# Optimization experiments

Measured on AMD Instinct MI355X. Metric: run time of the kernel, lower is better.

## Reference

```python
import jax, jax.numpy as jnp
import numpy as np

DIM = 2048
H = 16       # num_heads
HKV = 4      # num_kv_heads
HD = DIM // H  # head_dim = 128
REP = H // HKV
ROPE_BASE = 10000.0
QK_GAIN_INIT = 1.0
B, T = 4, 2048


def rms_norm(x):
    # F.rms_norm with eps=None -> machine eps of dtype, no weight
    eps = jnp.finfo(x.dtype).eps
    return x * jax.lax.rsqrt(jnp.mean(x * x, axis=-1, keepdims=True) + eps)


def apply_rotary_emb(x, cos, sin):
    # x: [B, h, T, HD]; cos/sin: [T, HD//2]
    h = x.shape[-1] // 2
    x1, x2 = x[..., :h], x[..., h:]
    return jnp.concatenate((x1 * cos + x2 * sin, -x1 * sin + x2 * cos), axis=-1)


def setup_inputs() -> dict:
    key = jax.random.key(0)
    ks = jax.random.split(key, 6)
    kv_dim = HKV * HD
    x = jax.random.normal(ks[0], (B, T, DIM), dtype=jnp.float32)
    Wq = jax.random.normal(ks[1], (DIM, DIM), dtype=jnp.float32) * 0.02
    Wk = jax.random.normal(ks[2], (kv_dim, DIM), dtype=jnp.float32) * 0.02
    Wv = jax.random.normal(ks[3], (kv_dim, DIM), dtype=jnp.float32) * 0.02
    Wproj = jax.random.normal(ks[4], (DIM, DIM), dtype=jnp.float32) * 0.02
    q_gain = jnp.full((H,), QK_GAIN_INIT, dtype=jnp.float32)
    return {"x": x, "Wq": Wq, "Wk": Wk, "Wv": Wv, "Wproj": Wproj, "q_gain": q_gain}


def reference(x, Wq, Wk, Wv, Wproj, q_gain):
    Bs, Ts, D = x.shape
    # QKV projections (bias-free Linear: x @ W.T)
    q = (x @ Wq.T).reshape(Bs, Ts, H, HD).transpose(0, 2, 1, 3)      # [B,H,T,HD]
    k = (x @ Wk.T).reshape(Bs, Ts, HKV, HD).transpose(0, 2, 1, 3)    # [B,HKV,T,HD]
    v = (x @ Wv.T).reshape(Bs, Ts, HKV, HD).transpose(0, 2, 1, 3)
    # RMSNorm over head_dim
    q, k = rms_norm(q), rms_norm(k)
    # rotary
    inv_freq = 1.0 / (ROPE_BASE ** (jnp.arange(0, HD, 2, dtype=jnp.float32) / HD))
    t = jnp.arange(Ts, dtype=jnp.float32)
    freqs = jnp.outer(t, inv_freq)  # [T, HD//2]
    cos, sin = jnp.cos(freqs), jnp.sin(freqs)
    q = apply_rotary_emb(q, cos, sin)
    k = apply_rotary_emb(k, cos, sin)
    # per-head query gain
    q = q * q_gain[None, :, None, None]
    # GQA attention without materializing repeated K/V
    qg = q.reshape(Bs, HKV, REP, Ts, HD)
    scale = 1.0 / jnp.sqrt(jnp.asarray(HD, dtype=q.dtype))
    scores = jnp.einsum('bgrtd,bgsd->bgrts', qg, k) * scale  # [B,HKV,REP,T,T]
    causal = jnp.tril(jnp.ones((Ts, Ts), dtype=bool))
    scores = jnp.where(causal, scores, jnp.finfo(scores.dtype).min)
    attn = jax.nn.softmax(scores, axis=-1)
    y = jnp.einsum('bgrts,bgsd->bgrtd', attn, v)              # [B,HKV,REP,T,HD]
    y = y.reshape(Bs, H, Ts, HD).transpose(0, 2, 1, 3).reshape(Bs, Ts, D)
    return y @ Wproj.T
```

## Files before the change

kernel.cpp:

```cpp
#include <hip/hip_runtime.h>
#include <stdint.h>

typedef unsigned short u16;
typedef __attribute__((ext_vector_type(4))) float f32x4;
typedef __attribute__((ext_vector_type(8))) __bf16 bf16x8;
typedef __attribute__((ext_vector_type(4))) u16 u16x4;
typedef __attribute__((ext_vector_type(8))) u16 u16x8;

#define T_SEQ 2048
#define NB 4
#define NH 16
#define NKV 4
#define HDIM 128
#define PSTR 72

__device__ __forceinline__ u16 f2bf(float f) {
  __bf16 h = (__bf16)f;
  return __builtin_bit_cast(u16, h);
}
__device__ __forceinline__ float bf2f(u16 u) {
  union { uint32_t u; float f; } v; v.u = ((uint32_t)u) << 16;
  return v.f;
}
__device__ __forceinline__ void gload16(const void* g, void* l) {
  __builtin_amdgcn_global_load_lds((const __attribute__((address_space(1))) void*)g,
                                   (__attribute__((address_space(3))) void*)l, 16, 0, 0);
}
__device__ __forceinline__ f32x4 mfma16(bf16x8 a, bf16x8 b, f32x4 c) {
  return __builtin_amdgcn_mfma_f32_16x16x32_bf16(a, b, c, 0, 0, 0);
}

__global__ __launch_bounds__(256) void cvt_bf16(const float* __restrict__ in,
                                                u16* __restrict__ out, int n) {
  int idx = blockIdx.x * 256 + threadIdx.x;
  int stride = gridDim.x * 256;
  for (int i = idx * 4; i < n; i += stride * 4) {
    f32x4 v = *(const f32x4*)(in + i);
    u16x4 o;
    o[0] = f2bf(v[0]); o[1] = f2bf(v[1]); o[2] = f2bf(v[2]); o[3] = f2bf(v[3]);
    *(u16x4*)(out + i) = o;
  }
}

template <int MODE>
__global__ __launch_bounds__(256) void gemm128p3(const u16* __restrict__ A,
                                                 const u16* __restrict__ Bt,
                                                 u16* __restrict__ q_o, u16* __restrict__ k_o,
                                                 u16* __restrict__ v_o, float* __restrict__ f_o,
                                                 int K, int nx, int cpx) {
  __shared__ __align__(16) u16 As3[3 * 128 * 32];
  __shared__ __align__(16) u16 Bs3[3 * 128 * 32];
  const int tid = threadIdx.x;
  const int l = tid & 63, w = tid >> 6;
  const int l15 = l & 15, g16 = l >> 4;
  const int wr = w >> 1, wc = w & 1;

  const int oid = blockIdx.x + nx * blockIdx.y;
  const int wid = (oid & 7) * cpx + (oid >> 3);
  const int m0 = (wid / nx) * 128, n0 = (wid % nx) * 128;

  f32x4 acc[4][4] = {};

  const int row0 = tid >> 2, row1 = 64 + (tid >> 2), cc = tid & 3;
  const int sc0 = cc ^ ((row0 >> 1) & 3), sc1 = cc ^ ((row1 >> 1) & 3);
  const u16* pA0 = A + (size_t)(m0 + row0) * K + sc0 * 8;
  const u16* pA1 = A + (size_t)(m0 + row1) * K + sc1 * 8;
  const u16* pB0 = Bt + (size_t)(n0 + row0) * K + sc0 * 8;
  const u16* pB1 = Bt + (size_t)(n0 + row1) * K + sc1 * 8;

#define STAGE(buf)                                                   \
  {                                                                  \
    char* ab = (char*)As3 + (buf) * 8192 + w * 1024;                 \
    char* bb = (char*)Bs3 + (buf) * 8192 + w * 1024;                 \
    gload16(pA0, ab);                                                \
    gload16(pA1, ab + 4096);                                         \
    gload16(pB0, bb);                                                \
    gload16(pB1, bb + 4096);                                         \
    pA0 += 32; pA1 += 32; pB0 += 32; pB1 += 32;                      \
  }

#define COMPUTE(buf)                                                 \
  {                                                                  \
    const u16* AsB = As3 + (buf) * 4096;                             \
    const u16* BsB = Bs3 + (buf) * 4096;                             \
    bf16x8 af[4], bfr[4];                                            \
    _Pragma("unroll")                                                \
    for (int mt = 0; mt < 4; ++mt) {                                 \
      int arow = wr * 64 + mt * 16 + l15;                            \
      af[mt] = *(const bf16x8*)&AsB[arow * 32 +                      \
                                    ((g16 ^ ((arow >> 1) & 3)) * 8)];\
    }                                                                \
    _Pragma("unroll")                                                \
    for (int nt = 0; nt < 4; ++nt) {                                 \
      int brow = wc * 64 + nt * 16 + l15;                            \
      bfr[nt] = *(const bf16x8*)&BsB[brow * 32 +                     \
                                     ((g16 ^ ((brow >> 1) & 3)) * 8)];\
    }                                                                \
    __builtin_amdgcn_s_setprio(1);                                   \
    _Pragma("unroll")                                                \
    for (int mt = 0; mt < 4; ++mt)                                   \
      _Pragma("unroll")                                              \
      for (int nt = 0; nt < 4; ++nt)                                 \
        acc[mt][nt] = mfma16(af[mt], bfr[nt], acc[mt][nt]);          \
    __builtin_amdgcn_s_setprio(0);                                   \
  }

  const int ntiles = K >> 5;
  STAGE(0);
  STAGE(1);
  asm volatile("s_waitcnt vmcnt(4)" ::: "memory");
  __builtin_amdgcn_s_barrier();

  int cur = 0, nxt = 2;
  for (int t = 0; t < ntiles; ++t) {
    const bool more2 = (t + 2 < ntiles);
    if (more2) STAGE(nxt);
    COMPUTE(cur);
    if (t + 1 < ntiles) {
      if (more2) {
        asm volatile("s_waitcnt vmcnt(4)" ::: "memory");
      } else {
        asm volatile("s_waitcnt vmcnt(0)" ::: "memory");
      }
      __builtin_amdgcn_s_barrier();
    }
    cur = (cur == 2) ? 0 : cur + 1;
    nxt = (nxt == 2) ? 0 : nxt + 1;
  }
#undef STAGE
#undef COMPUTE

#pragma unroll
  for (int mt = 0; mt < 4; ++mt) {
#pragma unroll
    for (int r = 0; r < 4; ++r) {
      int row = m0 + wr * 64 + mt * 16 + g16 * 4 + r;
#pragma unroll
      for (int nt = 0; nt < 4; ++nt) {
        int n = n0 + wc * 64 + nt * 16 + l15;
        float val = acc[mt][nt][r];
        if (MODE == 1) {
          f_o[(size_t)row * 2048 + n] = val;
        } else {
          int b = row >> 11, t = row & (T_SEQ - 1);
          u16 bv = f2bf(val);
          if (n < 2048) {
            int h = n >> 7, d = n & 127;
            q_o[((size_t)(b * NH + h) * T_SEQ + t) * HDIM + d] = bv;
          } else if (n < 2560) {
            int n2 = n - 2048; int h = n2 >> 7, d = n2 & 127;
            k_o[((size_t)(b * NKV + h) * T_SEQ + t) * HDIM + d] = bv;
          } else {
            int n2 = n - 2560; int h = n2 >> 7, d = n2 & 127;
            v_o[((size_t)(b * NKV + h) * T_SEQ + t) * HDIM + d] = bv;
          }
        }
      }
    }
  }
}

template <int MODE>
__global__ __launch_bounds__(512, 2) void gemm256(const u16* __restrict__ A,
                                                  const u16* __restrict__ Bt,
                                                  u16* __restrict__ q_o, u16* __restrict__ k_o,
                                                  u16* __restrict__ v_o, float* __restrict__ f_o,
                                                  int K, int ntn, int cpx) {
  __shared__ __align__(16) u16 As[2][256 * 64];
  __shared__ __align__(16) u16 Bs[2][256 * 64];
  const int tid = threadIdx.x;
  const int l = tid & 63, w = tid >> 6;
  const int l16 = l & 15, g16 = l >> 4;
  const int wr = w >> 2, wc = w & 3;

  const int oid = blockIdx.x;
  const int wid = (oid & 7) * cpx + (oid >> 3);
  const int m0 = (wid / ntn) * 256, n0 = (wid % ntn) * 256;

  f32x4 acc[8][4] = {};

  const int srow = tid >> 3, scc = tid & 7;
  const u16* pA[4];
  const u16* pB[4];
#pragma unroll
  for (int j = 0; j < 4; ++j) {
    int row = j * 64 + srow;
    int cc = scc ^ (row & 7);
    pA[j] = A + (size_t)(m0 + row) * K + cc * 8;
    pB[j] = Bt + (size_t)(n0 + row) * K + cc * 8;
  }

#define STAGE(buf)                                              \
  {                                                             \
    char* ab = (char*)As[buf] + w * 1024;                       \
    char* bb = (char*)Bs[buf] + w * 1024;                       \
    _Pragma("unroll")                                           \
    for (int j = 0; j < 4; ++j) {                               \
      gload16(pA[j], ab + j * 8192);                            \
      pA[j] += 64;                                              \
    }                                                           \
    _Pragma("unroll")                                           \
    for (int j = 0; j < 4; ++j) {                               \
      gload16(pB[j], bb + j * 8192);                            \
      pB[j] += 64;                                              \
    }                                                           \
  }

  const int ntk = K >> 6;
  STAGE(0);
  __syncthreads();

  for (int t = 0; t < ntk; ++t) {
    const int buf = t & 1;
    if (t + 1 < ntk) STAGE(buf ^ 1);
#pragma unroll
    for (int ks = 0; ks < 2; ++ks) {
      bf16x8 bfr[4];
#pragma unroll
      for (int nf = 0; nf < 4; ++nf) {
        int brow = wc * 64 + nf * 16 + l16;
        int slot = (ks * 4 + g16) ^ (brow & 7);
        bfr[nf] = *(const bf16x8*)&Bs[buf][brow * 64 + slot * 8];
      }
#pragma unroll
      for (int rh = 0; rh < 2; ++rh) {
        bf16x8 af[4];
#pragma unroll
        for (int f = 0; f < 4; ++f) {
          int arow = wr * 128 + rh * 64 + f * 16 + l16;
          int slot = (ks * 4 + g16) ^ (arow & 7);
          af[f] = *(const bf16x8*)&As[buf][arow * 64 + slot * 8];
        }
        __builtin_amdgcn_s_setprio(1);
#pragma unroll
        for (int f = 0; f < 4; ++f)
#pragma unroll
          for (int nf = 0; nf < 4; ++nf)
            acc[rh * 4 + f][nf] = mfma16(af[f], bfr[nf], acc[rh * 4 + f][nf]);
        __builtin_amdgcn_s_setprio(0);
      }
    }
    __syncthreads();
  }
#undef STAGE

#pragma unroll
  for (int rf = 0; rf < 8; ++rf) {
#pragma unroll
    for (int rr = 0; rr < 4; ++rr) {
      int row = m0 + wr * 128 + rf * 16 + g16 * 4 + rr;
#pragma unroll
      for (int nf = 0; nf < 4; ++nf) {
        int n = n0 + wc * 64 + nf * 16 + l16;
        float val = acc[rf][nf][rr];
        if (MODE == 1) {
          f_o[(size_t)row * 2048 + n] = val;
        } else {
          int b = row >> 11, t = row & (T_SEQ - 1);
          u16 bv = f2bf(val);
          if (n < 2048) {
            int h = n >> 7, d = n & 127;
            q_o[((size_t)(b * NH + h) * T_SEQ + t) * HDIM + d] = bv;
          } else if (n < 2560) {
            int n2 = n - 2048; int h = n2 >> 7, d = n2 & 127;
            k_o[((size_t)(b * NKV + h) * T_SEQ + t) * HDIM + d] = bv;
          } else {
            int n2 = n - 2560; int h = n2 >> 7, d = n2 & 127;
            v_o[((size_t)(b * NKV + h) * T_SEQ + t) * HDIM + d] = bv;
          }
        }
      }
    }
  }
}

__global__ __launch_bounds__(256) void rmsrope(u16* __restrict__ buf,
                                               const float* __restrict__ gains,
                                               int nheads, float fold, int useGain) {
  const int w = threadIdx.x >> 6, l = threadIdx.x & 63;
  const int rid = blockIdx.x * 4 + w;
  const int t = rid & (T_SEQ - 1);
  const int h = (rid >> 11) % nheads;
  u16* p = buf + (size_t)rid * HDIM;
  float x1 = bf2f(p[l]), x2 = bf2f(p[l + 64]);
  float ss = x1 * x1 + x2 * x2;
#pragma unroll
  for (int m = 32; m; m >>= 1) ss += __shfl_xor(ss, m, 64);
  float rn = rsqrtf(ss * (1.0f / 128.0f) + 1.1920928955078125e-7f);
  float g = useGain ? gains[h] * fold : fold;
  float sc = rn * g;
  float inv = exp2f(-(float)l * (13.287712379549449f / 64.0f));
  float ang = (float)t * inv;
  float s, c;
  __sincosf(ang, &s, &c);
  float o1 = (x1 * c + x2 * s) * sc;
  float o2 = (x2 * c - x1 * s) * sc;
  p[l] = f2bf(o1);
  p[l + 64] = f2bf(o2);
}

__global__ __launch_bounds__(256) void vtrans(const u16* __restrict__ in,
                                              u16* __restrict__ out) {
  __shared__ u16 tileT[64][PSTR];
  const int tid = threadIdx.x;
  const int t0 = blockIdx.x * 64, d0 = blockIdx.y * 64, bg = blockIdx.z;
  const int row = tid >> 2, c0 = (tid & 3) * 16;
  const u16* src = in + ((size_t)bg * T_SEQ + t0 + row) * HDIM + d0 + c0;
  u16x8 a = *(const u16x8*)src;
  u16x8 bb = *(const u16x8*)(src + 8);
#pragma unroll
  for (int j = 0; j < 8; ++j) {
    tileT[c0 + j][row] = a[j];
    tileT[c0 + 8 + j][row] = bb[j];
  }
  __syncthreads();
  u16* dst = out + ((size_t)bg * HDIM + d0 + row) * T_SEQ + t0 + c0;
  *(u16x8*)dst = *(const u16x8*)&tileT[row][c0];
  *(u16x8*)(dst + 8) = *(const u16x8*)&tileT[row][c0 + 8];
}

__global__ __launch_bounds__(256) void attn_fwd3(const u16* __restrict__ qb,
                                                 const u16* __restrict__ kb,
                                                 const u16* __restrict__ vtb,
                                                 u16* __restrict__ yb,
                                                 const float* __restrict__ gains) {
  __shared__ __align__(16) u16 Ks[64 * 128];
  __shared__ __align__(16) u16 Vs[128 * 64];
  __shared__ __align__(16) u16 Ps[4][32 * PSTR];

  const int tid = threadIdx.x, l = tid & 63, w = tid >> 6;
  const int l16 = l & 15, g16 = l >> 4;

  const int oid = blockIdx.x + 8 * blockIdx.y;
  const int wid = (oid & 7) * 64 + (oid >> 3);
  const int pair = wid & 7, bh = wid >> 3;
  const int b = bh >> 4, h = bh & 15, gr = h >> 2;

  const float Mh = 16.33f * fabsf(gains[h]) + 0.5f;
  const u16* kbase = kb + (size_t)(b * NKV + gr) * T_SEQ * HDIM;
  const u16* vtbase = vtb + (size_t)(b * NKV + gr) * HDIM * T_SEQ;

  for (int phase = 0; phase < 2; ++phase) {
    const int qt = phase ? (15 - pair) : pair;
    const int q0 = qt * 128 + w * 32;
    const int qhi = q0 + 31;

    bf16x8 qf[2][4];
    const u16* qbase = qb + ((size_t)bh * T_SEQ + q0) * HDIM;
#pragma unroll
    for (int nf = 0; nf < 2; ++nf)
#pragma unroll
      for (int s = 0; s < 4; ++s)
        qf[nf][s] = *(const bf16x8*)(qbase + (size_t)(nf * 16 + l16) * HDIM + s * 32 + g16 * 8);

    f32x4 oacc[2][8] = {};
    float den[2] = {0.f, 0.f};
    const int ntile = 2 * qt + 2;

    for (int kt = 0; kt < ntile; ++kt) {
#pragma unroll
      for (int r = 0; r < 4; ++r) {
        int c = r * 256 + tid;
        int row = c >> 4, c16 = c & 15;
        int sc = c16 ^ (row & 7);
        gload16(kbase + ((size_t)(kt * 64 + row)) * HDIM + sc * 8,
                (char*)Ks + (r * 256 + w * 64) * 16);
      }
#pragma unroll
      for (int r = 0; r < 4; ++r) {
        int c = r * 256 + tid;
        int row = c >> 3, c8 = c & 7;
        int sc = c8 ^ (row & 7);
        gload16(vtbase + (size_t)row * T_SEQ + kt * 64 + sc * 8,
                (char*)Vs + (r * 256 + w * 64) * 16);
      }
      __syncthreads();

      if (kt * 64 <= qhi) {
        f32x4 sacc[4][2] = {};
        __builtin_amdgcn_s_setprio(1);
#pragma unroll
        for (int mt = 0; mt < 4; ++mt) {
          int key = mt * 16 + l16;
#pragma unroll
          for (int s = 0; s < 4; ++s) {
            bf16x8 kf = *(const bf16x8*)&Ks[key * 128 + ((s * 4 + g16) ^ (key & 7)) * 8];
#pragma unroll
            for (int nf = 0; nf < 2; ++nf)
              sacc[mt][nf] = mfma16(kf, qf[nf][s], sacc[mt][nf]);
          }
        }
        __builtin_amdgcn_s_setprio(0);

        const bool diagcross = (kt * 64 + 63 > q0);
#pragma unroll
        for (int mt = 0; mt < 4; ++mt) {
          int keyb = kt * 64 + mt * 16 + g16 * 4;
#pragma unroll
          for (int nf = 0; nf < 2; ++nf) {
            u16x4 p4;
#pragma unroll
            for (int r = 0; r < 4; ++r) {
              float pv = exp2f(sacc[mt][nf][r] - Mh);
              if (diagcross && (keyb + r > q0 + nf * 16 + l16)) pv = 0.f;
              den[nf] += pv;
              p4[r] = f2bf(pv);
            }
            *(u16x4*)&Ps[w][(nf * 16 + l16) * PSTR + mt * 16 + g16 * 4] = p4;
          }
        }

        __builtin_amdgcn_s_setprio(1);
#pragma unroll
        for (int ks = 0; ks < 2; ++ks) {
          bf16x8 pa[2];
#pragma unroll
          for (int mq = 0; mq < 2; ++mq)
            pa[mq] = *(const bf16x8*)&Ps[w][(mq * 16 + l16) * PSTR + ks * 32 + g16 * 8];
#pragma unroll
          for (int dt = 0; dt < 8; ++dt) {
            int d = dt * 16 + l16;
            bf16x8 vv = *(const bf16x8*)&Vs[d * 64 + (((ks * 4 + g16) ^ (d & 7)) * 8)];
#pragma unroll
            for (int mq = 0; mq < 2; ++mq)
              oacc[mq][dt] = mfma16(pa[mq], vv, oacc[mq][dt]);
          }
        }
        __builtin_amdgcn_s_setprio(0);
      }
      __syncthreads();
    }

#pragma unroll
    for (int nf = 0; nf < 2; ++nf) {
      den[nf] += __shfl_xor(den[nf], 16, 64);
      den[nf] += __shfl_xor(den[nf], 32, 64);
    }
    float rden[2][4];
#pragma unroll
    for (int mq = 0; mq < 2; ++mq)
#pragma unroll
      for (int r = 0; r < 4; ++r)
        rden[mq][r] = 1.f / __shfl(den[mq], g16 * 4 + r, 64);

#pragma unroll
    for (int mq = 0; mq < 2; ++mq)
#pragma unroll
      for (int dt = 0; dt < 8; ++dt)
#pragma unroll
        for (int r = 0; r < 4; ++r) {
          int t = q0 + mq * 16 + g16 * 4 + r;
          int d = dt * 16 + l16;
          yb[(((size_t)b * T_SEQ + t) * NH + h) * HDIM + d] = f2bf(oacc[mq][dt][r] * rden[mq][r]);
        }
    __syncthreads();
  }
}

extern "C" void kernel_launch(void* const* d_in, const int* in_sizes, int n_in,
                              void* d_out, int out_size, void* d_ws, size_t ws_size,
                              hipStream_t stream) {
  const float* x = (const float*)d_in[0];
  const float* Wq = (const float*)d_in[1];
  const float* Wk = (const float*)d_in[2];
  const float* Wv = (const float*)d_in[3];
  const float* Wproj = (const float*)d_in[4];
  const float* qg = (const float*)d_in[5];
  float* out = (float*)d_out;

  u16* xbf = (u16*)d_ws;
  u16* Wqkv = xbf + (size_t)8192 * 2048;
  u16* Wpj = Wqkv + (size_t)3072 * 2048;
  u16* qbuf = Wpj + (size_t)2048 * 2048;
  u16* kbuf = qbuf + (size_t)8192 * 2048;
  u16* vbuf = kbuf + (size_t)2048 * 2048;
  u16* ybuf = xbf;
  u16* vtbuf = Wqkv;

  cvt_bf16<<<2048, 256, 0, stream>>>(x, xbf, 8192 * 2048);
  cvt_bf16<<<2048, 256, 0, stream>>>(Wq, Wqkv, 2048 * 2048);
  cvt_bf16<<<1024, 256, 0, stream>>>(Wk, Wqkv + (size_t)2048 * 2048, 512 * 2048);
  cvt_bf16<<<1024, 256, 0, stream>>>(Wv, Wqkv + (size_t)2560 * 2048, 512 * 2048);
  cvt_bf16<<<2048, 256, 0, stream>>>(Wproj, Wpj, 2048 * 2048);

  gemm128p3<0><<<dim3(24, 64), 256, 0, stream>>>(xbf, Wqkv, qbuf, kbuf, vbuf, nullptr,
                                                 2048, 24, 192);

  rmsrope<<<32768, 256, 0, stream>>>(qbuf, qg, NH,
                                     1.4426950408889634f / 11.313708498984761f, 1);
  rmsrope<<<8192, 256, 0, stream>>>(kbuf, nullptr, NKV, 1.0f, 0);
  vtrans<<<dim3(32, 2, 16), 256, 0, stream>>>(vbuf, vtbuf);

  attn_fwd3<<<dim3(8, 64), 256, 0, stream>>>(qbuf, kbuf, vtbuf, ybuf, qg);

  gemm256<1><<<256, 512, 0, stream>>>(ybuf, Wpj, nullptr, nullptr, nullptr, out, 2048, 8, 32);
}
```

Baseline: 361.6 us.

## Double-buffer K tiles and register-stage V loads in attention loop

Restructures the attention key loop into a two-stage software pipeline. K tiles alternate between two LDS buffers, and V tiles are prefetched into registers and written to LDS at the start of the next step, so the global loads for tile kt+1 are issued while tile kt is computed. The __syncthreads pairs become explicit barriers with waitcnt. This adds LDS use (an extra 16KB K buffer) and register pressure from the V staging registers, which may reduce occupancy.

```diff
diff --git a/kernel.cpp b/kernel.cpp
--- a/kernel.cpp
+++ b/kernel.cpp
@@ -319,12 +319,12 @@
   *(u16x8*)(dst + 8) = *(const u16x8*)&tileT[row][c0 + 8];
 }
 
-__global__ __launch_bounds__(256) void attn_fwd3(const u16* __restrict__ qb,
+__global__ __launch_bounds__(256) void attn_fwd5(const u16* __restrict__ qb,
                                                  const u16* __restrict__ kb,
                                                  const u16* __restrict__ vtb,
                                                  u16* __restrict__ yb,
                                                  const float* __restrict__ gains) {
-  __shared__ __align__(16) u16 Ks[64 * 128];
+  __shared__ __align__(16) u16 Ks[2][64 * 128];
   __shared__ __align__(16) u16 Vs[128 * 64];
   __shared__ __align__(16) u16 Ps[4][32 * PSTR];
 
@@ -340,6 +340,84 @@
   const u16* kbase = kb + (size_t)(b * NKV + gr) * T_SEQ * HDIM;
   const u16* vtbase = vtb + (size_t)(b * NKV + gr) * HDIM * T_SEQ;
 
+#define AK_STAGE(kbuf, ktile)                                              \
+  _Pragma("unroll")                                                        \
+  for (int r = 0; r < 4; ++r) {                                            \
+    int c = r * 256 + tid;                                                 \
+    int row = c >> 4;                                                      \
+    int sc = (c & 15) ^ (row & 7);                                         \
+    gload16(kbase + ((size_t)((ktile) * 64 + row)) * HDIM + sc * 8,        \
+            (char*)Ks[kbuf] + (r * 256 + w * 64) * 16);                    \
+  }
+#define AV_LOAD(vr, ktile)                                                 \
+  _Pragma("unroll")                                                        \
+  for (int r = 0; r < 4; ++r) {                                            \
+    int c = r * 256 + tid;                                                 \
+    int row = c >> 3;                                                      \
+    int sc = (c & 7) ^ (row & 7);                                          \
+    vr[r] = *(const u16x8*)(vtbase + (size_t)row * T_SEQ + (ktile) * 64 +  \
+                            sc * 8);                                       \
+  }
+#define AV_WRITE(vr)                                                       \
+  _Pragma("unroll")                                                        \
+  for (int r = 0; r < 4; ++r)                                              \
+    *(u16x8*)((char*)Vs + (r * 256 + tid) * 16) = vr[r];
+
+#define ATT_COMPUTE(ktv, kbuf)                                             \
+  if ((ktv) * 64 <= qhi) {                                                 \
+    f32x4 sacc[4][2] = {};                                                 \
+    __builtin_amdgcn_s_setprio(1);                                         \
+    _Pragma("unroll")                                                      \
+    for (int mt = 0; mt < 4; ++mt) {                                       \
+      int key = mt * 16 + l16;                                             \
+      _Pragma("unroll")                                                    \
+      for (int s = 0; s < 4; ++s) {                                        \
+        bf16x8 kf = *(const bf16x8*)&Ks[kbuf][key * 128 +                  \
+                                  (((s * 4 + g16) ^ (key & 7)) * 8)];      \
+        _Pragma("unroll")                                                  \
+        for (int nf = 0; nf < 2; ++nf)                                     \
+          sacc[mt][nf] = mfma16(kf, qf[nf][s], sacc[mt][nf]);              \
+      }                                                                    \
+    }                                                                      \
+    __builtin_amdgcn_s_setprio(0);                                         \
+    const bool diagcross = ((ktv) * 64 + 63 > q0);                         \
+    _Pragma("unroll")                                                      \
+    for (int mt = 0; mt < 4; ++mt) {                                       \
+      int keyb = (ktv) * 64 + mt * 16 + g16 * 4;                           \
+      _Pragma("unroll")                                                    \
+      for (int nf = 0; nf < 2; ++nf) {                                     \
+        u16x4 p4;                                                          \
+        _Pragma("unroll")                                                  \
+        for (int r = 0; r < 4; ++r) {                                      \
+          float pv = exp2f(sacc[mt][nf][r] - Mh);                          \
+          if (diagcross && (keyb + r > q0 + nf * 16 + l16)) pv = 0.f;      \
+          den[nf] += pv;                                                   \
+          p4[r] = f2bf(pv);                                                \
+        }                                                                  \
+        *(u16x4*)&Ps[w][(nf * 16 + l16) * PSTR + mt * 16 + g16 * 4] = p4;  \
+      }                                                                    \
+    }                                                                      \
+    __builtin_amdgcn_s_setprio(1);                                         \
+    _Pragma("unroll")                                                      \
+    for (int ks = 0; ks < 2; ++ks) {                                       \
+      bf16x8 pa[2];                                                        \
+      _Pragma("unroll")                                                    \
+      for (int mq = 0; mq < 2; ++mq)                                       \
+        pa[mq] = *(const bf16x8*)&Ps[w][(mq * 16 + l16) * PSTR +           \
+                                        ks * 32 + g16 * 8];                \
+      _Pragma("unroll")                                                    \
+      for (int dt = 0; dt < 8; ++dt) {                                     \
+        int d = dt * 16 + l16;                                             \
+        bf16x8 vv = *(const bf16x8*)&Vs[d * 64 +                           \
+                                  (((ks * 4 + g16) ^ (d & 7)) * 8)];       \
+        _Pragma("unroll")                                                  \
+        for (int mq = 0; mq < 2; ++mq)                                     \
+          oacc[mq][dt] = mfma16(pa[mq], vv, oacc[mq][dt]);                 \
+      }                                                                    \
+    }                                                                      \
+    __builtin_amdgcn_s_setprio(0);                                         \
+  }
+
   for (int phase = 0; phase < 2; ++phase) {
     const int qt = phase ? (15 - pair) : pair;
     const int q0 = qt * 128 + w * 32;
@@ -357,78 +435,30 @@
     float den[2] = {0.f, 0.f};
     const int ntile = 2 * qt + 2;
 
-    for (int kt = 0; kt < ntile; ++kt) {
-#pragma unroll
-      for (int r = 0; r < 4; ++r) {
-        int c = r * 256 + tid;
-        int row = c >> 4, c16 = c & 15;
-        int sc = c16 ^ (row & 7);
-        gload16(kbase + ((size_t)(kt * 64 + row)) * HDIM + sc * 8,
-                (char*)Ks + (r * 256 + w * 64) * 16);
+    u16x8 va[4], vb_[4];
+    AK_STAGE(0, 0);
+    AV_LOAD(va, 0);
+
+    for (int kt = 0; kt < ntile; kt += 2) {
+      __builtin_amdgcn_s_barrier();
+      asm volatile("s_waitcnt vmcnt(0)" ::: "memory");
+      AV_WRITE(va);
+      AK_STAGE(1, kt + 1);
+      AV_LOAD(vb_, kt + 1);
+      asm volatile("s_waitcnt lgkmcnt(0)" ::: "memory");
+      __builtin_amdgcn_s_barrier();
+      ATT_COMPUTE(kt, 0);
+
+      __builtin_amdgcn_s_barrier();
+      asm volatile("s_waitcnt vmcnt(0)" ::: "memory");
+      AV_WRITE(vb_);
+      if (kt + 2 < ntile) {
+        AK_STAGE(0, kt + 2);
+        AV_LOAD(va, kt + 2);
       }
-#pragma unroll
-      for (int r = 0; r < 4; ++r) {
-        int c = r * 256 + tid;
-        int row = c >> 3, c8 = c & 7;
-        int sc = c8 ^ (row & 7);
-        gload16(vtbase + (size_t)row * T_SEQ + kt * 64 + sc * 8,
-                (char*)Vs + (r * 256 + w * 64) * 16);
-      }
-      __syncthreads();
-
-      if (kt * 64 <= qhi) {
-        f32x4 sacc[4][2] = {};
-        __builtin_amdgcn_s_setprio(1);
-#pragma unroll
-        for (int mt = 0; mt < 4; ++mt) {
-          int key = mt * 16 + l16;
-#pragma unroll
-          for (int s = 0; s < 4; ++s) {
-            bf16x8 kf = *(const bf16x8*)&Ks[key * 128 + ((s * 4 + g16) ^ (key & 7)) * 8];
-#pragma unroll
-            for (int nf = 0; nf < 2; ++nf)
-              sacc[mt][nf] = mfma16(kf, qf[nf][s], sacc[mt][nf]);
-          }
-        }
-        __builtin_amdgcn_s_setprio(0);
-
-        const bool diagcross = (kt * 64 + 63 > q0);
-#pragma unroll
-        for (int mt = 0; mt < 4; ++mt) {
-          int keyb = kt * 64 + mt * 16 + g16 * 4;
-#pragma unroll
-          for (int nf = 0; nf < 2; ++nf) {
-            u16x4 p4;
-#pragma unroll
-            for (int r = 0; r < 4; ++r) {
-              float pv = exp2f(sacc[mt][nf][r] - Mh);
-              if (diagcross && (keyb + r > q0 + nf * 16 + l16)) pv = 0.f;
-              den[nf] += pv;
-              p4[r] = f2bf(pv);
-            }
-            *(u16x4*)&Ps[w][(nf * 16 + l16) * PSTR + mt * 16 + g16 * 4] = p4;
-          }
-        }
-
-        __builtin_amdgcn_s_setprio(1);
-#pragma unroll
-        for (int ks = 0; ks < 2; ++ks) {
-          bf16x8 pa[2];
-#pragma unroll
-          for (int mq = 0; mq < 2; ++mq)
-            pa[mq] = *(const bf16x8*)&Ps[w][(mq * 16 + l16) * PSTR + ks * 32 + g16 * 8];
-#pragma unroll
-          for (int dt = 0; dt < 8; ++dt) {
-            int d = dt * 16 + l16;
-            bf16x8 vv = *(const bf16x8*)&Vs[d * 64 + (((ks * 4 + g16) ^ (d & 7)) * 8)];
-#pragma unroll
-            for (int mq = 0; mq < 2; ++mq)
-              oacc[mq][dt] = mfma16(pa[mq], vv, oacc[mq][dt]);
-          }
-        }
-        __builtin_amdgcn_s_setprio(0);
-      }
-      __syncthreads();
+      asm volatile("s_waitcnt lgkmcnt(0)" ::: "memory");
+      __builtin_amdgcn_s_barrier();
+      ATT_COMPUTE(kt + 1, 1);
     }
 
 #pragma unroll
@@ -455,6 +485,10 @@
         }
     __syncthreads();
   }
+#undef AK_STAGE
+#undef AV_LOAD
+#undef AV_WRITE
+#undef ATT_COMPUTE
 }
 
 extern "C" void kernel_launch(void* const* d_in, const int* in_sizes, int n_in,
@@ -491,7 +525,7 @@
   rmsrope<<<8192, 256, 0, stream>>>(kbuf, nullptr, NKV, 1.0f, 0);
   vtrans<<<dim3(32, 2, 16), 256, 0, stream>>>(vbuf, vtbuf);
 
-  attn_fwd3<<<dim3(8, 64), 256, 0, stream>>>(qbuf, kbuf, vtbuf, ybuf, qg);
+  attn_fwd5<<<dim3(8, 64), 256, 0, stream>>>(qbuf, kbuf, vtbuf, ybuf, qg);
 
   gemm256<1><<<256, 512, 0, stream>>>(ybuf, Wpj, nullptr, nullptr, nullptr, out, 2048, 8, 32);
 }
```

Result: slower. 422.9 us (+16.9%).
